# Optimization experiments

Hardware: AMD Instinct MI355X
Metric: run time of the kernel (lower is better)

Reference implementation:

```python
import jax, jax.numpy as jnp
import numpy as np

B, V, T = 8, 25, 128
C, NH, DK = 256, 8, 32      # hidden_size = NH*DK; dv == dk (required by residual shapes)
DFF, IT = 1024, 4           # FFN hidden (d_in), num_layers
EPS_LN, EPS_BN, SLOPE = 1e-6, 1e-5, 0.01
SCALE = np.float32(1.0 / np.sqrt(DK))


def setup_inputs():
    ks = iter(jax.random.split(jax.random.key(0), 40))
    def w(shape, s=0.05):
        return jax.random.normal(next(ks), shape, jnp.float32) * s
    inp = {'data': jax.random.normal(next(ks), (B, C, V, T), jnp.float32)}
    inp['ln_g'] = jnp.ones((IT, C)); inp['ln_b'] = jnp.zeros((IT, C))
    for p in ('tj', 'tr'):
        for nm in ('q', 'k', 'v'):
            inp[p + '_w' + nm] = w((IT, C, C))
            inp[p + '_b' + nm] = jnp.zeros((IT, C))
        inp[p + '_bn_g'] = jnp.ones((IT, C)); inp[p + '_bn_b'] = jnp.zeros((IT, C))
        inp[p + '_w1'] = w((IT, DFF, C)); inp[p + '_b1'] = jnp.zeros((IT, DFF))
        inp[p + '_w2'] = w((IT, C, DFF)); inp[p + '_b2'] = jnp.zeros((IT, C))
        inp[p + '_fbn_g'] = jnp.ones((IT, C)); inp[p + '_fbn_b'] = jnp.zeros((IT, C))
    return inp


def _bn(x, g, b, axes):
    # train-mode BatchNorm: batch stats, biased variance; channel axis = 1
    m = x.mean(axes, keepdims=True)
    v = ((x - m) ** 2).mean(axes, keepdims=True)
    sh = [1] * x.ndim; sh[1] = -1
    return (x - m) * jax.lax.rsqrt(v + EPS_BN) * g.reshape(sh) + b.reshape(sh)


def _ffn(x, w1, b1, w2, b2, fg, fb):
    # PositionFeedForward on x: [N, C, L] -> [N, C, L]
    xt = jnp.swapaxes(x, 1, 2)                                   # [N, L, C]
    h = jax.nn.relu(jnp.einsum('nlc,fc->nlf', xt, w1) + b1)
    o = jnp.einsum('nlf,cf->nlc', h, w2) + b2 + xt               # residual
    return _bn(jnp.swapaxes(o, 1, 2), fg, fb, (0, 2))


def _tju(x, ax, wq, bq, wk, bk, wv, bv, bn_g, bn_b, w1, b1, w2, b2, fg, fb):
    # sliding-window (3) self-attn + 2 relay tokens; x: [N,C,T], ax: [N,C,2,T]
    N = x.shape[0]
    q = (jnp.einsum('oc,nct->not', wq, x) + bq[:, None]).reshape(N, NH, DK, T)
    k = (jnp.einsum('oc,nct->not', wk, x) + bk[:, None]).reshape(N, NH, DK, T)
    v = (jnp.einsum('oc,nct->not', wv, x) + bv[:, None]).reshape(N, NH, DK, T)
    kp = jnp.pad(k, ((0, 0), (0, 0), (0, 0), (1, 1)))
    vp = jnp.pad(v, ((0, 0), (0, 0), (0, 0), (1, 1)))
    kw = jnp.stack([kp[..., u:u + T] for u in range(3)], axis=3)  # [N,NH,DK,3,T]
    vw = jnp.stack([vp[..., u:u + T] for u in range(3)], axis=3)
    ak = (jnp.einsum('oc,ncat->noat', wk, ax) + bk[:, None, None]).reshape(N, NH, DK, 2, T)
    av = (jnp.einsum('oc,ncat->noat', wv, ax) + bv[:, None, None]).reshape(N, NH, DK, 2, T)
    kk = jnp.concatenate([kw, ak], axis=3)                        # [N,NH,DK,5,T]
    vv = jnp.concatenate([vw, av], axis=3)
    a = jax.nn.softmax(jnp.einsum('nhdt,nhdwt->nhwt', q, kk) * SCALE, axis=2)
    att = jnp.einsum('nhwt,nhdwt->nhdt', a, vv).reshape(N, C, T)
    ret = _bn(x + att, bn_g, bn_b, (0, 2))
    return _ffn(ret, w1, b1, w2, b2, fg, fb)


def _tru(r, y, wq, bq, wk, bk, wv, bv, bn_g, bn_b, w1, b1, w2, b2, fg, fb):
    # relay cross-attention; r: [N,C], y: [N,C,L]
    N, _, L = y.shape
    q = (r @ wq.T + bq).reshape(N, NH, DK)
    k = (jnp.einsum('oc,ncl->nol', wk, y) + bk[:, None]).reshape(N, NH, DK, L)
    v = (jnp.einsum('oc,ncl->nol', wv, y) + bv[:, None]).reshape(N, NH, DK, L)
    a = jax.nn.softmax(jnp.einsum('nhd,nhdl->nhl', q, k) * SCALE, axis=-1)
    att = jnp.einsum('nhl,nhdl->nhd', a, v).reshape(N, C)
    ret = _bn((r + att)[:, :, None], bn_g, bn_b, (0, 2))          # BN over batch
    return _ffn(ret, w1, b1, w2, b2, fg, fb)[:, :, 0]


def _forward(data, ln_g, ln_b, tj, tr):
    N = B * V
    embs = jnp.transpose(data, (0, 2, 1, 3)).reshape(N, C, T)
    nodes, relay = embs, embs.mean(2)                             # relay: [N,C]
    for i in range(IT):
        ax = jnp.concatenate([embs[:, :, None, :],
                              jnp.broadcast_to(relay[:, :, None, None], (N, C, 1, T))], axis=2)
        m = nodes.mean(1, keepdims=True)
        vv = nodes.var(1, keepdims=True)
        xln = (nodes - m) * jax.lax.rsqrt(vv + EPS_LN) * ln_g[i][None, :, None] + ln_b[i][None, :, None]
        nodes = jax.nn.leaky_relu(_tju(xln, ax, *[p[i] for p in tj]), SLOPE)
        y = jnp.concatenate([relay[:, :, None], nodes], axis=2)   # [N,C,T+1]
        relay = jax.nn.leaky_relu(_tru(relay, y, *[p[i] for p in tr]), SLOPE)
    return nodes.reshape(B, V, C, T)


def reference(data, ln_g, ln_b,
              tj_wq, tj_bq, tj_wk, tj_bk, tj_wv, tj_bv, tj_bn_g, tj_bn_b,
              tj_w1, tj_b1, tj_w2, tj_b2, tj_fbn_g, tj_fbn_b,
              tr_wq, tr_bq, tr_wk, tr_bk, tr_wv, tr_bv, tr_bn_g, tr_bn_b,
              tr_w1, tr_b1, tr_w2, tr_b2, tr_fbn_g, tr_fbn_b):
    tj = (tj_wq, tj_bq, tj_wk, tj_bk, tj_wv, tj_bv, tj_bn_g, tj_bn_b,
          tj_w1, tj_b1, tj_w2, tj_b2, tj_fbn_g, tj_fbn_b)
    tr = (tr_wq, tr_bq, tr_wk, tr_bk, tr_wv, tr_bv, tr_bn_g, tr_bn_b,
          tr_w1, tr_b1, tr_w2, tr_b2, tr_fbn_g, tr_fbn_b)
    return _forward(data, ln_g, ln_b, tj, tr)
```

## Files before the change

### kernel.cpp

```cpp
#include <hip/hip_runtime.h>
#include <cstddef>

#define BB   8
#define VV   25
#define TT   128
#define CC   256
#define NHH  8
#define DKK  32
#define DFFF 1024
#define ITER 4
#define NN   (BB*VV)
#define NT   (NN*TT)
#define LL1  (TT+1)
#define EPS_LN 1e-6f
#define EPS_BN 1e-5f
#define SLOPE  0.01f
#define SCALE_F 0.17677669529663687f

typedef unsigned short ushort_t;
typedef __attribute__((ext_vector_type(8))) short short8;
typedef __attribute__((ext_vector_type(4))) short short4_t;
typedef __attribute__((ext_vector_type(4))) float floatx4;

union U8 { short8 v; ushort_t u[8]; };

__device__ __forceinline__ float bf2f(ushort_t u) {
    union { unsigned int i; float f; } x; x.i = ((unsigned int)u) << 16; return x.f;
}
__device__ __forceinline__ ushort_t f2bf(float f) {
    union { float f; unsigned int i; } x; x.f = f;
    unsigned int r = x.i + 0x7FFFu + ((x.i >> 16) & 1u);
    return (ushort_t)(r >> 16);
}
__device__ __forceinline__ float2 bn_fin(float s, float ss) {
    float m = s * (1.0f/NT);
    float var = ss * (1.0f/NT) - m*m; if (var < 0.f) var = 0.f;
    return make_float2(m, rsqrtf(var + EPS_BN));
}

__device__ __forceinline__ void gl_lds16(const ushort_t* g, ushort_t* l) {
    __builtin_amdgcn_global_load_lds(
        (const __attribute__((address_space(1))) unsigned int*)g,
        (__attribute__((address_space(3))) unsigned int*)l,
        16, 0, 0);
}

__device__ __forceinline__ void ld32(const ushort_t* p, float* q) {
    #pragma unroll
    for (int c8 = 0; c8 < 4; c8++) {
        U8 u; u.v = *(const short8*)(p + c8*8);
        #pragma unroll
        for (int j = 0; j < 8; j++) q[c8*8+j] = bf2f(u.u[j]);
    }
}
__device__ __forceinline__ float dot32(const ushort_t* p, const float* q) {
    float s = 0.f;
    #pragma unroll
    for (int c8 = 0; c8 < 4; c8++) {
        U8 u; u.v = *(const short8*)(p + c8*8);
        #pragma unroll
        for (int j = 0; j < 8; j++) s += q[c8*8+j]*bf2f(u.u[j]);
    }
    return s;
}
__device__ __forceinline__ void acc32(const ushort_t* p, float e, float* av) {
    #pragma unroll
    for (int c8 = 0; c8 < 4; c8++) {
        U8 u; u.v = *(const short8*)(p + c8*8);
        #pragma unroll
        for (int j = 0; j < 8; j++) av[c8*8+j] += e*bf2f(u.u[j]);
    }
}

__global__ __launch_bounds__(256) void k_zero(float* __restrict__ p, int n)
{
    int i = blockIdx.x*256 + threadIdx.x;
    if (i < n) p[i] = 0.f;
}
__global__ __launch_bounds__(256) void k_cast2(const float* __restrict__ src,
    ushort_t* __restrict__ dst, int per, int dstride, int total)
{
    int i = blockIdx.x*256 + threadIdx.x;
    if (i < total) dst[(size_t)(i/per)*dstride + (i%per)] = f2bf(src[i]);
}
__global__ __launch_bounds__(256) void k_copy2(const float* __restrict__ src,
    float* __restrict__ dst, int per, int dstride, int total)
{
    int i = blockIdx.x*256 + threadIdx.x;
    if (i < total) dst[(size_t)(i/per)*dstride + (i%per)] = src[i];
}

__global__ __launch_bounds__(128) void k_embed(const float* __restrict__ data,
    float* __restrict__ nodesf, ushort_t* __restrict__ embs_bf, float* __restrict__ relay)
{
    __shared__ float tile[32][TT+1];
    int cc0 = blockIdx.x*32, n = blockIdx.y;
    int b = n / VV, v = n % VV, t = threadIdx.x;
    for (int cl = 0; cl < 32; cl++)
        tile[cl][t] = data[(((size_t)b*CC + cc0 + cl)*VV + v)*TT + t];
    __syncthreads();
    if (t < 32) {
        float s = 0.f;
        for (int tt = 0; tt < TT; tt++) s += tile[t][tt];
        relay[n*CC + cc0 + t] = s * (1.0f/TT);
    }
    #pragma unroll 8
    for (int it = 0; it < 32; it++) {
        int t_l = it*4 + (t >> 5), c_l = t & 31;
        float val = tile[c_l][t_l];
        size_t o = (size_t)(n*TT + t_l)*CC + cc0 + c_l;
        nodesf[o] = val;
        embs_bf[o] = f2bf(val);
    }
}

__global__ __launch_bounds__(256) void k_layernorm(float* __restrict__ x,
    ushort_t* __restrict__ outb, const float* __restrict__ g, const float* __restrict__ b)
{
    int wave = threadIdx.x >> 6, lane = threadIdx.x & 63;
    size_t base = (size_t)(blockIdx.x*4 + wave)*CC + lane*4;
    float4 v = *(float4*)&x[base];
    float s  = v.x + v.y + v.z + v.w;
    float ss = v.x*v.x + v.y*v.y + v.z*v.z + v.w*v.w;
    #pragma unroll
    for (int o = 32; o; o >>= 1) { s += __shfl_xor(s, o); ss += __shfl_xor(ss, o); }
    float m = s * (1.0f/CC);
    float var = ss * (1.0f/CC) - m*m; if (var < 0.f) var = 0.f;
    float rs = rsqrtf(var + EPS_LN);
    float4 gg = *(const float4*)&g[lane*4];
    float4 bb = *(const float4*)&b[lane*4];
    v.x = (v.x - m)*rs*gg.x + bb.x;
    v.y = (v.y - m)*rs*gg.y + bb.y;
    v.z = (v.z - m)*rs*gg.z + bb.z;
    v.w = (v.w - m)*rs*gg.w + bb.w;
    *(float4*)&x[base] = v;
    ushort_t o4[4] = {f2bf(v.x), f2bf(v.y), f2bf(v.z), f2bf(v.w)};
    *(short4_t*)&outb[base] = *(short4_t*)o4;
}

#define FL_RELU  1
#define FL_BF16  2
#define FL_RESBN 4

#define STAGE(SA, SB, T_) do {                                              \
    gl_lds16(aSrc[0] + (T_)*32, &SA[dstOff[0]]);                            \
    gl_lds16(bSrc[0] + (T_)*32, &SB[dstOff[0]]);                            \
    gl_lds16(aSrc[1] + (T_)*32, &SA[dstOff[1]]);                            \
    gl_lds16(bSrc[1] + (T_)*32, &SB[dstOff[1]]);                            \
    } while (0)

#define COMPUTE(SA, SB) do {                                                \
    short8 af_[4], bf_[4];                                                  \
    _Pragma("unroll")                                                       \
    for (int mi_ = 0; mi_ < 4; mi_++)                                       \
        af_[mi_] = *(const short8*)&SA[aOff[mi_]];                          \
    _Pragma("unroll")                                                       \
    for (int ni_ = 0; ni_ < 4; ni_++)                                       \
        bf_[ni_] = *(const short8*)&SB[bOff[ni_]];                          \
    _Pragma("unroll")                                                       \
    for (int mi_ = 0; mi_ < 4; mi_++)                                       \
        _Pragma("unroll")                                                   \
        for (int ni_ = 0; ni_ < 4; ni_++)                                   \
            acc[mi_][ni_] = __builtin_amdgcn_mfma_f32_16x16x32_bf16(        \
                bf_[ni_], af_[mi_], acc[mi_][ni_], 0, 0, 0);                \
    } while (0)

#define PHASE(CA, CB, PA, PB, T_) do {                                      \
    if ((T_) + 2 < NK) STAGE(PA, PB, (T_) + 2);                             \
    COMPUTE(CA, CB);                                                        \
    if ((T_) + 1 < NK) {                                                    \
        __builtin_amdgcn_sched_barrier(0);                                  \
        if ((T_) + 2 < NK)                                                  \
            asm volatile("s_waitcnt vmcnt(4) lgkmcnt(0)" ::: "memory");     \
        else                                                                \
            asm volatile("s_waitcnt vmcnt(0) lgkmcnt(0)" ::: "memory");     \
        __builtin_amdgcn_s_barrier();                                       \
        __builtin_amdgcn_sched_barrier(0);                                  \
    }                                                                       \
    } while (0)

template<int K, int STATS>
__global__ __launch_bounds__(256) void k_gemm_mfma(
    const ushort_t* A, const ushort_t* B, const float* bias,
    const float* rx, const float* __restrict__ rawms,
    const float* __restrict__ bng, const float* __restrict__ bnb,
    float* outf, ushort_t* outb, int ostride, int ntiles_n, int flags,
    const ushort_t* A2, const ushort_t* B2, const float* bias2,
    ushort_t* outb2, int ostride2, int ntiles_n2,
    float* stats_acc)
{
    __shared__ ushort_t sA0[128*32];
    __shared__ ushort_t sB0[128*32];
    __shared__ ushort_t sA1[128*32];
    __shared__ ushort_t sB1[128*32];
    __shared__ ushort_t sA2[128*32];
    __shared__ ushort_t sB2[128*32];
    const int pid = blockIdx.x;
    const int xcd = pid & 7, idx = pid >> 3;
    const int ntile_tot = ntiles_n + ntiles_n2;
    const int nt_i = idx % ntile_tot;
    const int m0 = (xcd*25 + idx/ntile_tot) * 128;
    const ushort_t* Ap;  const ushort_t* Bp;  const float* biasp;
    ushort_t* outbp;  int ostridep, n0;
    if (nt_i < ntiles_n) {
        Ap = A;  Bp = B;  biasp = bias;  outbp = outb;
        ostridep = ostride;  n0 = nt_i*128;
    } else {
        Ap = A2; Bp = B2; biasp = bias2; outbp = outb2;
        ostridep = ostride2; n0 = (nt_i - ntiles_n)*128;
    }
    const int tid = threadIdx.x;
    const int lane = tid & 63, wave = tid >> 6;
    const int wm = (wave & 1) * 64, wn = (wave >> 1) * 64;
    const int fr = lane >> 4, fc = lane & 15;

    const ushort_t* aSrc[2];
    const ushort_t* bSrc[2];
    int dstOff[2];
    #pragma unroll
    for (int j = 0; j < 2; j++) {
        int s = wave*128 + j*64 + lane;
        int row = s >> 2;
        int kcs = ((s & 3) - (row >> 1)) & 3;
        aSrc[j] = Ap + (size_t)(m0 + row)*K + kcs*8;
        bSrc[j] = Bp + (size_t)(n0 + row)*K + kcs*8;
        dstOff[j] = (wave*128 + j*64)*8;
    }
    int aOff[4], bOff[4];
    #pragma unroll
    for (int mi = 0; mi < 4; mi++) {
        int row = wm + mi*16 + fc;
        aOff[mi] = row*32 + (((fr + (row >> 1)) & 3) * 8);
    }
    #pragma unroll
    for (int ni = 0; ni < 4; ni++) {
        int row = wn + ni*16 + fc;
        bOff[ni] = row*32 + (((fr + (row >> 1)) & 3) * 8);
    }

    floatx4 acc[4][4];
    #pragma unroll
    for (int i = 0; i < 4; i++)
        #pragma unroll
        for (int j = 0; j < 4; j++) acc[i][j] = (floatx4){0.f,0.f,0.f,0.f};

    constexpr int NK = K >> 5;
    STAGE(sA0, sB0, 0);
    if (NK > 1) STAGE(sA1, sB1, 1);
    __builtin_amdgcn_sched_barrier(0);
    if (NK > 1) asm volatile("s_waitcnt vmcnt(4)" ::: "memory");
    else        asm volatile("s_waitcnt vmcnt(0)" ::: "memory");
    __builtin_amdgcn_s_barrier();
    __builtin_amdgcn_sched_barrier(0);

    #pragma unroll
    for (int tb = 0; tb < NK; tb += 3) {
        PHASE(sA0, sB0, sA2, sB2, tb);
        if (tb + 1 < NK) PHASE(sA1, sB1, sA0, sB0, tb + 1);
        if (tb + 2 < NK) PHASE(sA2, sB2, sA1, sB1, tb + 2);
    }

    float st[4][4], sst[4][4];
    if constexpr (STATS) {
        #pragma unroll
        for (int a = 0; a < 4; a++)
            #pragma unroll
            for (int b2_ = 0; b2_ < 4; b2_++) { st[a][b2_] = 0.f; sst[a][b2_] = 0.f; }
    }
    #pragma unroll
    for (int ni = 0; ni < 4; ni++) {
        int nb = n0 + wn + ni*16 + fr*4;
        float4 bias4 = *(const float4*)&biasp[nb];
        float bm[4] = {0,0,0,0}, bs[4] = {0,0,0,0}, bb2[4] = {0,0,0,0};
        if (flags & FL_RESBN) {
            float4 s1 = *(const float4*)&rawms[nb];
            float4 s2 = *(const float4*)&rawms[CC + nb];
            float4 g4 = *(const float4*)&bng[nb];
            float4 b4 = *(const float4*)&bnb[nb];
            float2 f0 = bn_fin(s1.x, s2.x); float2 f1 = bn_fin(s1.y, s2.y);
            float2 f2 = bn_fin(s1.z, s2.z); float2 f3 = bn_fin(s1.w, s2.w);
            bm[0]=f0.x; bm[1]=f1.x; bm[2]=f2.x; bm[3]=f3.x;
            bs[0]=f0.y*g4.x; bs[1]=f1.y*g4.y; bs[2]=f2.y*g4.z; bs[3]=f3.y*g4.w;
            bb2[0]=b4.x; bb2[1]=b4.y; bb2[2]=b4.z; bb2[3]=b4.w;
        }
        float bia[4] = {bias4.x, bias4.y, bias4.z, bias4.w};
        #pragma unroll
        for (int mi = 0; mi < 4; mi++) {
            int m = m0 + wm + mi*16 + fc;
            size_t idx2 = (size_t)m*ostridep + nb;
            float vals[4];
            #pragma unroll
            for (int r = 0; r < 4; r++) vals[r] = acc[mi][ni][r] + bia[r];
            if (flags & FL_RESBN) {
                float4 rx4 = *(const float4*)&rx[idx2];
                float rxa[4] = {rx4.x, rx4.y, rx4.z, rx4.w};
                #pragma unroll
                for (int r = 0; r < 4; r++)
                    vals[r] += (rxa[r] - bm[r])*bs[r] + bb2[r];
            }
            if (flags & FL_RELU)
                #pragma unroll
                for (int r = 0; r < 4; r++) vals[r] = fmaxf(vals[r], 0.f);
            if constexpr (STATS) {
                #pragma unroll
                for (int r = 0; r < 4; r++) {
                    st[ni][r] += vals[r];
                    sst[ni][r] += vals[r]*vals[r];
                }
            }
            if (flags & FL_BF16) {
                ushort_t o4[4] = {f2bf(vals[0]), f2bf(vals[1]),
                                  f2bf(vals[2]), f2bf(vals[3])};
                *(short4_t*)&outbp[idx2] = *(short4_t*)o4;
            } else {
                float4 ov = make_float4(vals[0], vals[1], vals[2], vals[3]);
                *(float4*)&outf[idx2] = ov;
            }
        }
    }
    if constexpr (STATS) {
        #pragma unroll
        for (int ni = 0; ni < 4; ni++)
            #pragma unroll
            for (int r = 0; r < 4; r++) {
                float s_ = st[ni][r], ss_ = sst[ni][r];
                #pragma unroll
                for (int msk = 1; msk < 16; msk <<= 1) {
                    s_  += __shfl_xor(s_,  msk);
                    ss_ += __shfl_xor(ss_, msk);
                }
                st[ni][r] = s_; sst[ni][r] = ss_;
            }
        if (fc == 0) {
            #pragma unroll
            for (int ni = 0; ni < 4; ni++)
                #pragma unroll
                for (int r = 0; r < 4; r++) {
                    int ch = n0 + wn + ni*16 + fr*4 + r;
                    atomicAdd(&stats_acc[ch],      st[ni][r]);
                    atomicAdd(&stats_acc[CC + ch], sst[ni][r]);
                }
        }
    }
}

__global__ __launch_bounds__(256) void k_sgemm(
    const float* __restrict__ W, const float* __restrict__ X,
    const float* __restrict__ bias, const float* __restrict__ res,
    float* __restrict__ out, int K, int OUT, int do_relu)
{
    __shared__ float sW[16][260];
    __shared__ float sX[16][260];
    int o0 = blockIdx.x*16, n0 = blockIdx.y*16;
    int tx = threadIdx.x, ty = threadIdx.y;
    int tid = ty*16 + tx;
    float acc0 = 0.f, acc1 = 0.f;
    for (int kc = 0; kc < K; kc += 256) {
        #pragma unroll
        for (int j = 0; j < 4; j++) {
            int lin = tid + j*256;
            int row = lin >> 6, c4 = (lin & 63)*4;
            *(float4*)&sW[row][c4] = *(const float4*)&W[(size_t)(o0+row)*K + kc + c4];
            float4 xv = make_float4(0.f,0.f,0.f,0.f);
            if (n0 + row < NN) xv = *(const float4*)&X[(size_t)(n0+row)*K + kc + c4];
            *(float4*)&sX[row][c4] = xv;
        }
        __syncthreads();
        #pragma unroll 8
        for (int k4 = 0; k4 < 64; k4 += 2) {
            float4 w0 = *(const float4*)&sW[tx][k4*4];
            float4 x0 = *(const float4*)&sX[ty][k4*4];
            float4 w1 = *(const float4*)&sW[tx][k4*4+4];
            float4 x1 = *(const float4*)&sX[ty][k4*4+4];
            acc0 += w0.x*x0.x + w0.y*x0.y + w0.z*x0.z + w0.w*x0.w;
            acc1 += w1.x*x1.x + w1.y*x1.y + w1.z*x1.z + w1.w*x1.w;
        }
        __syncthreads();
    }
    float accv = acc0 + acc1;
    int o = o0 + tx, n = n0 + ty;
    if (n < NN) {
        float val = accv + bias[o];
        if (res) val += res[(size_t)n*OUT + o];
        if (do_relu) val = fmaxf(val, 0.f);
        out[(size_t)n*OUT + o] = val;
    }
}

__global__ __launch_bounds__(128) void k_attn_tj(
    const ushort_t* __restrict__ qkv, const ushort_t* __restrict__ ekv,
    const float* __restrict__ rel, const float* __restrict__ xln,
    float* __restrict__ out, float* __restrict__ accum)
{
    __shared__ float svals[128][33];
    int t = threadIdx.x, h = blockIdx.x, n = blockIdx.y;
    int nt = n*TT + t;
    const ushort_t* qp = qkv + (size_t)nt*768 + h*32;
    const ushort_t* kp = qp + 256;
    const ushort_t* vp = qp + 512;
    const ushort_t* ep = ekv + (size_t)nt*512 + h*32;
    const float*    rp = rel + n*1280 + h*32;

    float qv[32];
    ld32(qp, qv);
    float s0 = 0.f, s1, s2 = 0.f, s3, s4 = 0.f;
    s1 = dot32(kp, qv);
    s3 = dot32(ep, qv);
    #pragma unroll
    for (int j = 0; j < 8; j++) {
        float4 rv4 = *(const float4*)&rp[j*4];
        s4 += qv[j*4]*rv4.x + qv[j*4+1]*rv4.y + qv[j*4+2]*rv4.z + qv[j*4+3]*rv4.w;
    }
    if (t > 0)    s0 = dot32(kp - 768, qv);
    if (t < TT-1) s2 = dot32(kp + 768, qv);

    s0 *= SCALE_F; s1 *= SCALE_F; s2 *= SCALE_F; s3 *= SCALE_F; s4 *= SCALE_F;
    float mx = fmaxf(fmaxf(fmaxf(s0, s1), fmaxf(s2, s3)), s4);
    float e0 = expf(s0-mx), e1 = expf(s1-mx), e2 = expf(s2-mx), e3 = expf(s3-mx), e4 = expf(s4-mx);
    float inv = 1.f/(e0+e1+e2+e3+e4);
    e0 *= inv; e1 *= inv; e2 *= inv; e3 *= inv; e4 *= inv;

    float av[32];
    #pragma unroll
    for (int d = 0; d < 32; d++) av[d] = 0.f;
    acc32(vp, e1, av);
    acc32(ep + 256, e3, av);
    if (t > 0)    acc32(vp - 768, e0, av);
    if (t < TT-1) acc32(vp + 768, e2, av);
    #pragma unroll
    for (int j = 0; j < 8; j++) {
        float4 rv4 = *(const float4*)&rp[256 + j*4];
        av[j*4] += e4*rv4.x; av[j*4+1] += e4*rv4.y; av[j*4+2] += e4*rv4.z; av[j*4+3] += e4*rv4.w;
    }
    const float* xp = xln + (size_t)nt*CC + h*32;
    float* op = out + (size_t)nt*CC + h*32;
    #pragma unroll
    for (int j = 0; j < 8; j++) {
        float4 xv = *(const float4*)&xp[j*4];
        float4 ov;
        ov.x = xv.x + av[j*4]; ov.y = xv.y + av[j*4+1];
        ov.z = xv.z + av[j*4+2]; ov.w = xv.w + av[j*4+3];
        *(float4*)&op[j*4] = ov;
        svals[t][j*4+0] = ov.x; svals[t][j*4+1] = ov.y;
        svals[t][j*4+2] = ov.z; svals[t][j*4+3] = ov.w;
    }
    __syncthreads();
    if (t < 64) {
        int ch = t & 31, seg = t >> 5;
        float s = 0.f, ss = 0.f;
        for (int r = 0; r < 64; r++) {
            float v = svals[seg*64 + r][ch];
            s += v; ss += v*v;
        }
        atomicAdd(&accum[h*32 + ch], s);
        atomicAdd(&accum[CC + h*32 + ch], ss);
    }
}

__global__ __launch_bounds__(256) void k_bn_apply_raw(const float* __restrict__ x,
    const float* __restrict__ acc, const float* __restrict__ g, const float* __restrict__ b,
    ushort_t* __restrict__ outb)
{
    size_t base = ((size_t)blockIdx.x*256 + threadIdx.x)*4;
    int c0 = (int)(base & (CC-1));
    float4 v  = *(const float4*)&x[base];
    float4 a1 = *(const float4*)&acc[c0];
    float4 a2 = *(const float4*)&acc[CC + c0];
    float4 g4 = *(const float4*)&g[c0];
    float4 b4 = *(const float4*)&b[c0];
    float vals[4] = {v.x,v.y,v.z,v.w};
    float s1v[4] = {a1.x,a1.y,a1.z,a1.w};
    float s2v[4] = {a2.x,a2.y,a2.z,a2.w};
    float gg[4] = {g4.x,g4.y,g4.z,g4.w};
    float bb[4] = {b4.x,b4.y,b4.z,b4.w};
    ushort_t o4[4];
    #pragma unroll
    for (int j = 0; j < 4; j++) {
        float2 f = bn_fin(s1v[j], s2v[j]);
        o4[j] = f2bf((vals[j] - f.x)*f.y*gg[j] + bb[j]);
    }
    *(short4_t*)&outb[base] = *(short4_t*)o4;
}

__global__ __launch_bounds__(256) void k_bn_ln(const float* __restrict__ x,
    const float* __restrict__ acc, const float* __restrict__ fg, const float* __restrict__ fb,
    const float* __restrict__ lg, const float* __restrict__ lb,
    float* __restrict__ xlnf, ushort_t* __restrict__ xlnb, ushort_t* __restrict__ nodesb)
{
    int wave = threadIdx.x >> 6, lane = threadIdx.x & 63;
    int c0 = lane*4;
    size_t base = (size_t)(blockIdx.x*4 + wave)*CC + c0;
    float4 v  = *(const float4*)&x[base];
    float4 a1 = *(const float4*)&acc[c0];
    float4 a2 = *(const float4*)&acc[CC + c0];
    float4 g4 = *(const float4*)&fg[c0];
    float4 b4 = *(const float4*)&fb[c0];
    float vals[4] = {v.x,v.y,v.z,v.w};
    float s1v[4] = {a1.x,a1.y,a1.z,a1.w};
    float s2v[4] = {a2.x,a2.y,a2.z,a2.w};
    float gg[4] = {g4.x,g4.y,g4.z,g4.w};
    float bb[4] = {b4.x,b4.y,b4.z,b4.w};
    ushort_t nb4[4];
    #pragma unroll
    for (int j = 0; j < 4; j++) {
        float2 f = bn_fin(s1v[j], s2v[j]);
        float vv = (vals[j] - f.x)*f.y*gg[j] + bb[j];
        vv = vv > 0.f ? vv : SLOPE*vv;
        vals[j] = vv;
        nb4[j] = f2bf(vv);
    }
    *(short4_t*)&nodesb[base] = *(short4_t*)nb4;
    float s  = vals[0]+vals[1]+vals[2]+vals[3];
    float ss = vals[0]*vals[0]+vals[1]*vals[1]+vals[2]*vals[2]+vals[3]*vals[3];
    #pragma unroll
    for (int o = 32; o; o >>= 1) { s += __shfl_xor(s, o); ss += __shfl_xor(ss, o); }
    float m = s * (1.0f/CC);
    float var = ss * (1.0f/CC) - m*m; if (var < 0.f) var = 0.f;
    float rs = rsqrtf(var + EPS_LN);
    float4 lg4 = *(const float4*)&lg[c0];
    float4 lb4 = *(const float4*)&lb[c0];
    float lgv[4] = {lg4.x,lg4.y,lg4.z,lg4.w};
    float lbv[4] = {lb4.x,lb4.y,lb4.z,lb4.w};
    float4 xo;
    ushort_t xb4[4];
    float t0 = (vals[0]-m)*rs*lgv[0] + lbv[0];
    float t1 = (vals[1]-m)*rs*lgv[1] + lbv[1];
    float t2 = (vals[2]-m)*rs*lgv[2] + lbv[2];
    float t3 = (vals[3]-m)*rs*lgv[3] + lbv[3];
    xo.x = t0; xo.y = t1; xo.z = t2; xo.w = t3;
    xb4[0]=f2bf(t0); xb4[1]=f2bf(t1); xb4[2]=f2bf(t2); xb4[3]=f2bf(t3);
    *(float4*)&xlnf[base] = xo;
    *(short4_t*)&xlnb[base] = *(short4_t*)xb4;
}

__global__ __launch_bounds__(256) void k_bn_out_t(const float* __restrict__ x,
    const float* __restrict__ acc, const float* __restrict__ g, const float* __restrict__ b,
    float* __restrict__ out)
{
    __shared__ float tile[64][65];
    int nt0 = blockIdx.x*64, c0 = blockIdx.y*64;
    int w = threadIdx.x >> 6, lane = threadIdx.x & 63;
    int n = nt0 >> 7, t0 = nt0 & 127;
    int c = c0 + lane;
    float2 f = bn_fin(acc[c], acc[CC + c]);
    float gg = f.y*g[c], mm = f.x, bb = b[c];
    #pragma unroll
    for (int it = 0; it < 16; it++) {
        int tok = it*4 + w;
        float v = x[(size_t)(nt0 + tok)*CC + c];
        v = (v - mm)*gg + bb;
        v = v > 0.f ? v : SLOPE*v;
        tile[tok][lane] = v;
    }
    __syncthreads();
    #pragma unroll
    for (int it = 0; it < 16; it++) {
        int c_l = it*4 + w;
        out[(size_t)(n*CC + c0 + c_l)*TT + t0 + lane] = tile[lane][c_l];
    }
}

__global__ __launch_bounds__(64) void k_bn_relay(const float* __restrict__ x,
    float* __restrict__ out, const float* __restrict__ g, const float* __restrict__ b, int leaky)
{
    int c = blockIdx.x, tid = threadIdx.x;
    float s = 0.f, ss = 0.f;
    for (int n = tid; n < NN; n += 64) { float v = x[(size_t)n*CC + c]; s += v; ss += v*v; }
    for (int off = 32; off; off >>= 1) { s += __shfl_down(s, off); ss += __shfl_down(ss, off); }
    float S = __shfl(s, 0), SS = __shfl(ss, 0);
    float m = S / NN;
    float var = SS / NN - m*m; if (var < 0.f) var = 0.f;
    float rs = rsqrtf(var + EPS_BN);
    float gg = g[c]*rs, bb = b[c];
    for (int n = tid; n < NN; n += 64) {
        float v = (x[(size_t)n*CC + c] - m)*gg + bb;
        if (leaky) v = v > 0.f ? v : SLOPE*v;
        out[(size_t)n*CC + c] = v;
    }
}

__global__ __launch_bounds__(64) void k_attn_tr(
    const float* __restrict__ rel, const float* __restrict__ ykv,
    const float* __restrict__ relay, float* __restrict__ out)
{
    int h = blockIdx.x, n = blockIdx.y, tid = threadIdx.x;
    __shared__ float sc[LL1];
    __shared__ float red[64][33];
    float q0[32];
    const float* qp = rel + (size_t)n*1280 + 1024 + h*32;
    #pragma unroll
    for (int j = 0; j < 8; j++) {
        float4 v = *(const float4*)&qp[j*4];
        q0[j*4] = v.x; q0[j*4+1] = v.y; q0[j*4+2] = v.z; q0[j*4+3] = v.w;
    }
    for (int l = tid; l < LL1; l += 64) {
        const float* kp = (l == 0) ? (rel + (size_t)n*1280 + 512 + h*32)
                                   : (ykv + (size_t)(n*TT + l-1)*512 + h*32);
        float s = 0.f;
        #pragma unroll
        for (int j = 0; j < 8; j++) {
            float4 v = *(const float4*)&kp[j*4];
            s += q0[j*4]*v.x + q0[j*4+1]*v.y + q0[j*4+2]*v.z + q0[j*4+3]*v.w;
        }
        sc[l] = s * SCALE_F;
    }
    __syncthreads();
    float mx = -1e30f;
    for (int l = tid; l < LL1; l += 64) mx = fmaxf(mx, sc[l]);
    for (int off = 32; off; off >>= 1) mx = fmaxf(mx, __shfl_xor(mx, off));
    float sum = 0.f;
    for (int l = tid; l < LL1; l += 64) { float e = expf(sc[l]-mx); sc[l] = e; sum += e; }
    for (int off = 32; off; off >>= 1) sum += __shfl_xor(sum, off);
    __syncthreads();
    float av[32];
    #pragma unroll
    for (int d = 0; d < 32; d++) av[d] = 0.f;
    for (int l = tid; l < LL1; l += 64) {
        float e = sc[l];
        const float* vp = (l == 0) ? (rel + (size_t)n*1280 + 768 + h*32)
                                   : (ykv + (size_t)(n*TT + l-1)*512 + 256 + h*32);
        #pragma unroll
        for (int j = 0; j < 8; j++) {
            float4 v = *(const float4*)&vp[j*4];
            av[j*4] += e*v.x; av[j*4+1] += e*v.y; av[j*4+2] += e*v.z; av[j*4+3] += e*v.w;
        }
    }
    #pragma unroll
    for (int d = 0; d < 32; d++) red[tid][d] = av[d];
    __syncthreads();
    if (tid < 32) {
        float a = 0.f;
        for (int k = 0; k < 64; k++) a += red[k][tid];
        a /= sum;
        int idx = n*CC + h*32 + tid;
        out[idx] = relay[idx] + a;
    }
}

extern "C" void kernel_launch(void* const* d_in, const int* in_sizes, int n_in,
                              void* d_out, int out_size, void* d_ws, size_t ws_size,
                              hipStream_t stream)
{
    const float* data    = (const float*)d_in[0];
    const float* ln_g    = (const float*)d_in[1];
    const float* ln_b    = (const float*)d_in[2];
    const float* tj_wq   = (const float*)d_in[3];
    const float* tj_bq   = (const float*)d_in[4];
    const float* tj_wk   = (const float*)d_in[5];
    const float* tj_bk   = (const float*)d_in[6];
    const float* tj_wv   = (const float*)d_in[7];
    const float* tj_bv   = (const float*)d_in[8];
    const float* tj_bn_g = (const float*)d_in[9];
    const float* tj_bn_b = (const float*)d_in[10];
    const float* tj_w1   = (const float*)d_in[11];
    const float* tj_b1   = (const float*)d_in[12];
    const float* tj_w2   = (const float*)d_in[13];
    const float* tj_b2   = (const float*)d_in[14];
    const float* tj_fbn_g= (const float*)d_in[15];
    const float* tj_fbn_b= (const float*)d_in[16];
    const float* tr_wq   = (const float*)d_in[17];
    const float* tr_bq   = (const float*)d_in[18];
    const float* tr_wk   = (const float*)d_in[19];
    const float* tr_bk   = (const float*)d_in[20];
    const float* tr_wv   = (const float*)d_in[21];
    const float* tr_bv   = (const float*)d_in[22];
    const float* tr_bn_g = (const float*)d_in[23];
    const float* tr_bn_b = (const float*)d_in[24];
    const float* tr_w1   = (const float*)d_in[25];
    const float* tr_b1   = (const float*)d_in[26];
    const float* tr_w2   = (const float*)d_in[27];
    const float* tr_b2   = (const float*)d_in[28];
    const float* tr_fbn_g= (const float*)d_in[29];
    const float* tr_fbn_b= (const float*)d_in[30];

    const size_t SZ = (size_t)NT*CC;
    const size_t SZ_NC = (size_t)NN*CC;

    float* ws = (float*)d_ws;
    size_t off = 0;
    auto alloc = [&](size_t nf) { float* p = ws + off; off += nf; return p; };
    float*    nodesf  = alloc(SZ);
    float*    sbuf    = alloc(SZ);
    float*    P1      = alloc(SZ*5/2);
    ushort_t* xs_bf   = (ushort_t*)alloc(SZ/2);
    ushort_t* embs_bf = (ushort_t*)alloc(SZ/2);
    ushort_t* nb_bf   = (ushort_t*)alloc(SZ/2);
    float* accs   = alloc(8*512);
    float* relayA = alloc(SZ_NC);
    float* relayB = alloc(SZ_NC);
    float* rel    = alloc((size_t)NN*1280);
    float* ret0   = alloc(SZ_NC);
    float* rret   = alloc(SZ_NC);
    float* ro     = alloc(SZ_NC);
    float* rh     = alloc((size_t)NN*DFFF);
    ushort_t* wqkv_bf  = (ushort_t*)alloc((size_t)ITER*768*CC/2);
    ushort_t* wkvtr_bf = (ushort_t*)alloc((size_t)ITER*512*CC/2);
    ushort_t* w1_bf    = (ushort_t*)alloc((size_t)ITER*DFFF*CC/2);
    ushort_t* w2_bf    = (ushort_t*)alloc((size_t)ITER*DFFF*CC/2);
    float* wrel  = alloc((size_t)ITER*1280*CC);
    float* brel  = alloc((size_t)ITER*1280);
    float* bqkv  = alloc((size_t)ITER*768);
    float* bkvtr = alloc((size_t)ITER*512);
    (void)ws_size; (void)in_sizes; (void)n_in; (void)out_size;

    ushort_t* qkv_tm = (ushort_t*)P1;
    ushort_t* ekv_tm = qkv_tm + 3*SZ;
    ushort_t* h_us   = (ushort_t*)P1;
    float*    ykv_f  = P1;

    const int TCC = ITER*CC*CC, TFF = ITER*DFFF*CC;
    k_zero<<<16, 256, 0, stream>>>(accs, 8*512);
    k_cast2<<<(TCC+255)/256, 256, 0, stream>>>(tj_wq, wqkv_bf,          65536, 196608, TCC);
    k_cast2<<<(TCC+255)/256, 256, 0, stream>>>(tj_wk, wqkv_bf +  65536, 65536, 196608, TCC);
    k_cast2<<<(TCC+255)/256, 256, 0, stream>>>(tj_wv, wqkv_bf + 131072, 65536, 196608, TCC);
    k_cast2<<<(TCC+255)/256, 256, 0, stream>>>(tr_wk, wkvtr_bf,         65536, 131072, TCC);
    k_cast2<<<(TCC+255)/256, 256, 0, stream>>>(tr_wv, wkvtr_bf + 65536, 65536, 131072, TCC);
    k_cast2<<<(TFF+255)/256, 256, 0, stream>>>(tj_w1, w1_bf, TFF, TFF, TFF);
    k_cast2<<<(TFF+255)/256, 256, 0, stream>>>(tj_w2, w2_bf, TFF, TFF, TFF);
    k_copy2<<<(ITER*256+255)/256, 256, 0, stream>>>(tj_bq, bqkv,       256, 768, ITER*256);
    k_copy2<<<(ITER*256+255)/256, 256, 0, stream>>>(tj_bk, bqkv + 256, 256, 768, ITER*256);
    k_copy2<<<(ITER*256+255)/256, 256, 0, stream>>>(tj_bv, bqkv + 512, 256, 768, ITER*256);
    k_copy2<<<(ITER*256+255)/256, 256, 0, stream>>>(tr_bk, bkvtr,      256, 512, ITER*256);
    k_copy2<<<(ITER*256+255)/256, 256, 0, stream>>>(tr_bv, bkvtr+256,  256, 512, ITER*256);
    k_copy2<<<(TCC+255)/256, 256, 0, stream>>>(tj_wk, wrel,          65536, 327680, TCC);
    k_copy2<<<(TCC+255)/256, 256, 0, stream>>>(tj_wv, wrel +  65536, 65536, 327680, TCC);
    k_copy2<<<(TCC+255)/256, 256, 0, stream>>>(tr_wk, wrel + 131072, 65536, 327680, TCC);
    k_copy2<<<(TCC+255)/256, 256, 0, stream>>>(tr_wv, wrel + 196608, 65536, 327680, TCC);
    k_copy2<<<(TCC+255)/256, 256, 0, stream>>>(tr_wq, wrel + 262144, 65536, 327680, TCC);
    k_copy2<<<(ITER*256+255)/256, 256, 0, stream>>>(tj_bk, brel,        256, 1280, ITER*256);
    k_copy2<<<(ITER*256+255)/256, 256, 0, stream>>>(tj_bv, brel +  256, 256, 1280, ITER*256);
    k_copy2<<<(ITER*256+255)/256, 256, 0, stream>>>(tr_bk, brel +  512, 256, 1280, ITER*256);
    k_copy2<<<(ITER*256+255)/256, 256, 0, stream>>>(tr_bv, brel +  768, 256, 1280, ITER*256);
    k_copy2<<<(ITER*256+255)/256, 256, 0, stream>>>(tr_bq, brel + 1024, 256, 1280, ITER*256);

    k_embed<<<dim3(8, NN), 128, 0, stream>>>(data, nodesf, embs_bf, relayA);
    k_layernorm<<<NT/4, 256, 0, stream>>>(nodesf, xs_bf, ln_g, ln_b);

    float* relay = relayA;
    float* relay_next = relayB;
    dim3 sb16(16, 16);

    for (int i = 0; i < ITER; i++) {
        const size_t woff = (size_t)i*DFFF*CC;
        float* accA = accs + i*1024;
        float* accB = accs + i*1024 + 512;

        k_sgemm<<<dim3((i == ITER-1) ? 32 : 80, 13), sb16, 0, stream>>>(
            wrel + (size_t)i*1280*CC, relay, brel + i*1280, nullptr, rel, CC, 1280, 0);

        k_gemm_mfma<256,0><<<200*10, 256, 0, stream>>>(
            xs_bf, wqkv_bf + (size_t)i*768*CC, bqkv + i*768,
            nullptr, nullptr, nullptr, nullptr,
            nullptr, qkv_tm, 768, 6, FL_BF16,
            embs_bf, wqkv_bf + (size_t)i*768*CC + 65536, bqkv + i*768 + 256,
            ekv_tm, 512, 4, nullptr);

        k_attn_tj<<<dim3(NHH, NN), 128, 0, stream>>>(qkv_tm, ekv_tm, rel, nodesf, sbuf, accA);

        k_bn_apply_raw<<<SZ/1024, 256, 0, stream>>>(
            sbuf, accA, tj_bn_g + i*CC, tj_bn_b + i*CC, xs_bf);

        k_gemm_mfma<256,0><<<200*8, 256, 0, stream>>>(
            xs_bf, w1_bf + woff, tj_b1 + i*DFFF, nullptr, nullptr, nullptr, nullptr,
            nullptr, h_us, DFFF, 8, FL_RELU | FL_BF16,
            nullptr, nullptr, nullptr, nullptr, 0, 0, nullptr);
        k_gemm_mfma<1024,1><<<200*2, 256, 0, stream>>>(
            h_us, w2_bf + woff, tj_b2 + i*CC, sbuf, accA, tj_bn_g + i*CC, tj_bn_b + i*CC,
            sbuf, nullptr, CC, 2, FL_RESBN,
            nullptr, nullptr, nullptr, nullptr, 0, 0, accB);

        if (i == ITER-1) {
            k_bn_out_t<<<dim3(NT/64, CC/64), 256, 0, stream>>>(
                sbuf, accB, tj_fbn_g + i*CC, tj_fbn_b + i*CC, (float*)d_out);
            break;
        }
        k_bn_ln<<<NT/4, 256, 0, stream>>>(
            sbuf, accB, tj_fbn_g + i*CC, tj_fbn_b + i*CC,
            ln_g + (i+1)*CC, ln_b + (i+1)*CC, nodesf, xs_bf, nb_bf);

        k_gemm_mfma<256,0><<<200*4, 256, 0, stream>>>(
            nb_bf, wkvtr_bf + (size_t)i*512*CC, bkvtr + i*512,
            nullptr, nullptr, nullptr, nullptr,
            ykv_f, nullptr, 512, 4, 0,
            nullptr, nullptr, nullptr, nullptr, 0, 0, nullptr);

        k_attn_tr<<<dim3(NHH, NN), 64, 0, stream>>>(rel, ykv_f, relay, ret0);
        k_bn_relay<<<CC, 64, 0, stream>>>(ret0, rret, tr_bn_g + i*CC, tr_bn_b + i*CC, 0);

        k_sgemm<<<dim3(DFFF/16, (NN+15)/16), sb16, 0, stream>>>(
            tr_w1 + woff, rret, tr_b1 + i*DFFF, nullptr, rh, CC, DFFF, 1);
        k_sgemm<<<dim3(16, (NN+15)/16), sb16, 0, stream>>>(
            tr_w2 + woff, rh, tr_b2 + i*CC, rret, ro, DFFF, CC, 0);
        k_bn_relay<<<CC, 64, 0, stream>>>(ro, relay_next, tr_fbn_g + i*CC, tr_fbn_b + i*CC, 1);

        float* tmp = relay; relay = relay_next; relay_next = tmp;
    }
}
```

Measured before the change: 1.275 ms.

## Store QKV/KV projections head-major and split BN stats into separate kernel

The MFMA GEMM epilogue gains a head-major output layout flag, so Q/K/V and relay K/V are written as [head][token][32] instead of token-major rows. The attention kernels read neighbouring tokens at a 32-element stride, which makes per-thread loads across a wavefront contiguous. The per-block BatchNorm statistics reduction with atomics is moved out of the tj attention kernel into a new token-major stats kernel. That removes the LDS staging and barrier from attention, at the cost of an extra launch and an extra read of the attention output.

```diff
diff --git a/kernel.cpp b/kernel.cpp
--- a/kernel.cpp
+++ b/kernel.cpp
@@ -141,6 +141,7 @@
 #define FL_RELU  1
 #define FL_BF16  2
 #define FL_RESBN 4
+#define FL_HM    8
 
 #define STAGE(SA, SB, T_) do {                                              \
     gl_lds16(aSrc[0] + (T_)*32, &SA[dstOff[0]]);                            \
@@ -284,10 +285,12 @@
             bb2[0]=b4.x; bb2[1]=b4.y; bb2[2]=b4.z; bb2[3]=b4.w;
         }
         float bia[4] = {bias4.x, bias4.y, bias4.z, bias4.w};
+        size_t hm_base = ((size_t)(nb >> 5) * NT) * 32 + (nb & 31);
         #pragma unroll
         for (int mi = 0; mi < 4; mi++) {
             int m = m0 + wm + mi*16 + fc;
-            size_t idx2 = (size_t)m*ostridep + nb;
+            size_t idx2 = (flags & FL_HM) ? hm_base + (size_t)m*32
+                                          : (size_t)m*ostridep + nb;
             float vals[4];
             #pragma unroll
             for (int r = 0; r < 4; r++) vals[r] = acc[mi][ni][r] + bia[r];
@@ -390,15 +393,15 @@
 __global__ __launch_bounds__(128) void k_attn_tj(
     const ushort_t* __restrict__ qkv, const ushort_t* __restrict__ ekv,
     const float* __restrict__ rel, const float* __restrict__ xln,
-    float* __restrict__ out, float* __restrict__ accum)
-{
-    __shared__ float svals[128][33];
+    float* __restrict__ out)
+{
     int t = threadIdx.x, h = blockIdx.x, n = blockIdx.y;
     int nt = n*TT + t;
-    const ushort_t* qp = qkv + (size_t)nt*768 + h*32;
-    const ushort_t* kp = qp + 256;
-    const ushort_t* vp = qp + 512;
-    const ushort_t* ep = ekv + (size_t)nt*512 + h*32;
+    const ushort_t* qp = qkv + ((size_t)h*NT       + nt)*32;
+    const ushort_t* kp = qkv + ((size_t)(8+h)*NT   + nt)*32;
+    const ushort_t* vp = qkv + ((size_t)(16+h)*NT  + nt)*32;
+    const ushort_t* ep = ekv + ((size_t)h*NT       + nt)*32;
+    const ushort_t* evp= ekv + ((size_t)(8+h)*NT   + nt)*32;
     const float*    rp = rel + n*1280 + h*32;
 
     float qv[32];
@@ -411,8 +414,8 @@
         float4 rv4 = *(const float4*)&rp[j*4];
         s4 += qv[j*4]*rv4.x + qv[j*4+1]*rv4.y + qv[j*4+2]*rv4.z + qv[j*4+3]*rv4.w;
     }
-    if (t > 0)    s0 = dot32(kp - 768, qv);
-    if (t < TT-1) s2 = dot32(kp + 768, qv);
+    if (t > 0)    s0 = dot32(kp - 32, qv);
+    if (t < TT-1) s2 = dot32(kp + 32, qv);
 
     s0 *= SCALE_F; s1 *= SCALE_F; s2 *= SCALE_F; s3 *= SCALE_F; s4 *= SCALE_F;
     float mx = fmaxf(fmaxf(fmaxf(s0, s1), fmaxf(s2, s3)), s4);
@@ -424,9 +427,9 @@
     #pragma unroll
     for (int d = 0; d < 32; d++) av[d] = 0.f;
     acc32(vp, e1, av);
-    acc32(ep + 256, e3, av);
-    if (t > 0)    acc32(vp - 768, e0, av);
-    if (t < TT-1) acc32(vp + 768, e2, av);
+    acc32(evp, e3, av);
+    if (t > 0)    acc32(vp - 32, e0, av);
+    if (t < TT-1) acc32(vp + 32, e2, av);
     #pragma unroll
     for (int j = 0; j < 8; j++) {
         float4 rv4 = *(const float4*)&rp[256 + j*4];
@@ -441,20 +444,29 @@
         ov.x = xv.x + av[j*4]; ov.y = xv.y + av[j*4+1];
         ov.z = xv.z + av[j*4+2]; ov.w = xv.w + av[j*4+3];
         *(float4*)&op[j*4] = ov;
-        svals[t][j*4+0] = ov.x; svals[t][j*4+1] = ov.y;
-        svals[t][j*4+2] = ov.z; svals[t][j*4+3] = ov.w;
-    }
+    }
+}
+
+__global__ __launch_bounds__(256) void k_bnstats_tm(const float* __restrict__ x,
+    float* __restrict__ accum)
+{
+    __shared__ float lds[8][256];
+    int w = threadIdx.x >> 6, lane = threadIdx.x & 63;
+    size_t base = (size_t)blockIdx.x*TT*CC;
+    float s[4] = {0,0,0,0}, ss[4] = {0,0,0,0};
+    for (int tok = w; tok < TT; tok += 4) {
+        float4 v = *(const float4*)&x[base + (size_t)tok*CC + lane*4];
+        s[0] += v.x; s[1] += v.y; s[2] += v.z; s[3] += v.w;
+        ss[0] += v.x*v.x; ss[1] += v.y*v.y; ss[2] += v.z*v.z; ss[3] += v.w*v.w;
+    }
+    #pragma unroll
+    for (int j = 0; j < 4; j++) { lds[w][lane*4+j] = s[j]; lds[4+w][lane*4+j] = ss[j]; }
     __syncthreads();
-    if (t < 64) {
-        int ch = t & 31, seg = t >> 5;
-        float s = 0.f, ss = 0.f;
-        for (int r = 0; r < 64; r++) {
-            float v = svals[seg*64 + r][ch];
-            s += v; ss += v*v;
-        }
-        atomicAdd(&accum[h*32 + ch], s);
-        atomicAdd(&accum[CC + h*32 + ch], ss);
-    }
+    int c = threadIdx.x;
+    float ps  = lds[0][c]+lds[1][c]+lds[2][c]+lds[3][c];
+    float pss = lds[4][c]+lds[5][c]+lds[6][c]+lds[7][c];
+    atomicAdd(&accum[c], ps);
+    atomicAdd(&accum[CC + c], pss);
 }
 
 __global__ __launch_bounds__(256) void k_bn_apply_raw(const float* __restrict__ x,
@@ -595,7 +607,7 @@
     }
     for (int l = tid; l < LL1; l += 64) {
         const float* kp = (l == 0) ? (rel + (size_t)n*1280 + 512 + h*32)
-                                   : (ykv + (size_t)(n*TT + l-1)*512 + h*32);
+                                   : (ykv + ((size_t)h*NT + n*TT + l-1)*32);
         float s = 0.f;
         #pragma unroll
         for (int j = 0; j < 8; j++) {
@@ -618,7 +630,7 @@
     for (int l = tid; l < LL1; l += 64) {
         float e = sc[l];
         const float* vp = (l == 0) ? (rel + (size_t)n*1280 + 768 + h*32)
-                                   : (ykv + (size_t)(n*TT + l-1)*512 + 256 + h*32);
+                                   : (ykv + ((size_t)(8+h)*NT + n*TT + l-1)*32);
         #pragma unroll
         for (int j = 0; j < 8; j++) {
             float4 v = *(const float4*)&vp[j*4];
@@ -751,12 +763,13 @@
         k_gemm_mfma<256,0><<<200*10, 256, 0, stream>>>(
             xs_bf, wqkv_bf + (size_t)i*768*CC, bqkv + i*768,
             nullptr, nullptr, nullptr, nullptr,
-            nullptr, qkv_tm, 768, 6, FL_BF16,
+            nullptr, qkv_tm, 768, 6, FL_BF16 | FL_HM,
             embs_bf, wqkv_bf + (size_t)i*768*CC + 65536, bqkv + i*768 + 256,
             ekv_tm, 512, 4, nullptr);
 
-        k_attn_tj<<<dim3(NHH, NN), 128, 0, stream>>>(qkv_tm, ekv_tm, rel, nodesf, sbuf, accA);
-
+        k_attn_tj<<<dim3(NHH, NN), 128, 0, stream>>>(qkv_tm, ekv_tm, rel, nodesf, sbuf);
+
+        k_bnstats_tm<<<NN, 256, 0, stream>>>(sbuf, accA);
         k_bn_apply_raw<<<SZ/1024, 256, 0, stream>>>(
             sbuf, accA, tj_bn_g + i*CC, tj_bn_b + i*CC, xs_bf);
 
@@ -781,7 +794,7 @@
         k_gemm_mfma<256,0><<<200*4, 256, 0, stream>>>(
             nb_bf, wkvtr_bf + (size_t)i*512*CC, bkvtr + i*512,
             nullptr, nullptr, nullptr, nullptr,
-            ykv_f, nullptr, 512, 4, 0,
+            ykv_f, nullptr, 512, 4, FL_HM,
             nullptr, nullptr, nullptr, nullptr, 0, 0, nullptr);
 
         k_attn_tr<<<dim3(NHH, NN), 64, 0, stream>>>(rel, ykv_f, relay, ret0);
```

Measured after the change: 1.213 ms. -4.9%, faster.
